# Optimization experiments

Measured on AMD Instinct MI355X. Metric: run time of the kernel, lower is better.

Reference implementation:

```python
import jax, jax.numpy as jnp
import numpy as np

B, N, K, F, O = 8, 65536, 9, 32, 64


def setup_inputs() -> dict:
    key = jax.random.key(0)
    k1, k2, k3, k4, k5 = jax.random.split(key, 5)
    x = jax.random.normal(k1, (B, N, F), dtype=jnp.float32)
    neighbor_index = jax.random.randint(k2, (B, N, K), 0, N)
    t_vertex = jax.random.randint(k3, (N,), 0, N)  # unused in forward, kept for signature fidelity
    v = jnp.ones((N, 8), dtype=jnp.float32) / 8.0
    adjweight = jnp.broadcast_to(jnp.eye(K, dtype=jnp.float32)[None], (8, K, K))
    W = jax.random.normal(k4, (O, K * F), dtype=jnp.float32) * 0.02
    b = jnp.zeros((O,), dtype=jnp.float32)
    return {"x": x, "t_vertex": t_vertex, "neighbor_index": neighbor_index,
            "v": v, "adjweight": adjweight, "W": W, "b": b}


def reference(x, t_vertex, neighbor_index, v, adjweight, W, b):
    bsize, num_pts, feats = x.shape
    num_neighbor = neighbor_index.shape[-1]
    # gather neighbor features per batch: [B, N, K, F]
    x_neighbors = jax.vmap(lambda xb, ib: xb[ib])(x, neighbor_index)
    # per-point learned adjacency: [N, K, K]
    adjw = jnp.einsum('ns,skt->nkt', v, adjweight)
    # apply adjacency: [B, N, K, F] (t replaces k)
    xn = jnp.einsum('bnkf,nkt->bntf', x_neighbors, adjw)
    xn = jax.nn.elu(xn.reshape(bsize, num_pts, num_neighbor * feats))
    out = jax.nn.elu(jnp.einsum('bnd,od->bno', xn, W) + b)
    # zero out last (padding) vertex
    mask = jnp.ones((1, num_pts, 1), dtype=out.dtype).at[0, -1, 0].set(0.0)
    return out * mask
```

## Files before the change

kernel.cpp:

```cpp
#include <hip/hip_runtime.h>
#include <hip/hip_bf16.h>

#define NLOG 16
#define NN 65536
#define KK 9
#define FF 32
#define OO 64
#define DD 288
#define WSTR 296
#define CHUNK 64
#define THREADS 256
#define GRID 2048
#define NBLOCKS 1024
#define TOTALP (8 * NN)
#define NCHUNKS (TOTALP / CHUNK)
#define RA_STRIDE 72
#define RB_STRIDE 10
#define NB_STRIDE 10
#define AJW 88

#define XB (TOTALP * FF / 8 / THREADS)
#define AB (NN * KK / THREADS)
#define NB (TOTALP / THREADS)
#define WB (OO * DD / THREADS)

typedef float f32x4 __attribute__((ext_vector_type(4)));
typedef float f32x2 __attribute__((ext_vector_type(2)));
typedef unsigned int u32x4 __attribute__((ext_vector_type(4)));
typedef short s16x8 __attribute__((ext_vector_type(8)));
typedef short s16x4 __attribute__((ext_vector_type(4)));

static __device__ __forceinline__ short f2bf(float f) {
    union { __hip_bfloat16 h; short s; } u;
    u.h = __float2bfloat16(f);
    return u.s;
}

static __device__ __forceinline__ void bf2f2(unsigned int p, float& lo, float& hi) {
    union { unsigned int u; float f; } a, b;
    a.u = p << 16;
    b.u = p & 0xFFFF0000u;
    lo = a.f; hi = b.f;
}
static __device__ __forceinline__ float bf1(unsigned short s) {
    union { unsigned int u; float f; } a;
    a.u = ((unsigned int)s) << 16;
    return a.f;
}

static __device__ __forceinline__ float elu1(float x) {
    float e = __expf(fminf(x, 0.f)) - 1.f;
    return x > 0.f ? x : e;
}

__global__ __launch_bounds__(THREADS) void precvt(
    const float* __restrict__ x, unsigned short* __restrict__ xbf,
    const float* __restrict__ v, const float* __restrict__ aw,
    unsigned short* __restrict__ recA, unsigned short* __restrict__ recB,
    const int* __restrict__ nbr, unsigned short* __restrict__ nb16,
    const float* __restrict__ W, unsigned short* __restrict__ wbf)
{
    const int bid = blockIdx.x;
    if (bid < XB) {
        const size_t i = ((size_t)bid * THREADS + threadIdx.x) * 8;
        const f32x4 a = *(const f32x4*)(x + i);
        const f32x4 b = *(const f32x4*)(x + i + 4);
        s16x8 p;
        p[0] = f2bf(a.x); p[1] = f2bf(a.y); p[2] = f2bf(a.z); p[3] = f2bf(a.w);
        p[4] = f2bf(b.x); p[5] = f2bf(b.y); p[6] = f2bf(b.z); p[7] = f2bf(b.w);
        *(s16x8*)(xbf + i) = p;
    } else if (bid < XB + AB) {
        const int e = (bid - XB) * THREADS + threadIdx.x;
        const int n = e / KK;
        const int t = e - n * KK;
        const float* vr = v + n * 8;
        short o[8];
        float s8 = 0.f;
        #pragma unroll
        for (int k = 0; k < KK; ++k) {
            float s = 0.f;
            #pragma unroll
            for (int si = 0; si < 8; ++si)
                s += vr[si] * aw[si * 81 + k * 9 + t];
            if (k < 8) o[k] = f2bf(s); else s8 = s;
        }
        *(s16x8*)(recA + (size_t)n * RA_STRIDE + t * 8) = *(s16x8*)o;
        recB[(size_t)n * RB_STRIDE + t] = (unsigned short)f2bf(s8);
        if (t == 0) recB[(size_t)n * RB_STRIDE + 9] = 0;
    } else if (bid < XB + AB + NB) {
        const int p = (bid - XB - AB) * THREADS + threadIdx.x;
        const int* s = nbr + (size_t)p * KK;
        int r[KK];
        #pragma unroll
        for (int k = 0; k < KK; ++k) r[k] = s[k];
        unsigned int* d = (unsigned int*)(nb16 + (size_t)p * NB_STRIDE);
        #pragma unroll
        for (int j = 0; j < 4; ++j)
            d[j] = ((unsigned)r[2*j] & 0xFFFFu) | ((unsigned)r[2*j+1] << 16);
        d[4] = (unsigned)r[8] & 0xFFFFu;
    } else {
        const int i = (bid - XB - AB - NB) * THREADS + threadIdx.x;
        wbf[i] = (unsigned short)f2bf(W[i]);
    }
}

__global__ __launch_bounds__(THREADS, 2) void paiconv_main(
    const unsigned short* __restrict__ xbf,
    const unsigned short* __restrict__ nb16,
    const unsigned short* __restrict__ recA,
    const unsigned short* __restrict__ recB,
    const unsigned short* __restrict__ wbf,
    const float* __restrict__ bias,
    float* __restrict__ out)
{
    __shared__ short Wl[OO * WSTR];
    __shared__ unsigned short AJ[CHUNK * AJW];

    const int tid  = threadIdx.x;
    const int lane = tid & 63;
    const int wid  = tid >> 6;
    const int l15  = lane & 15;
    const int fg   = lane >> 4;
    const int fo   = fg * 8;
    const int pl   = wid * 16 + l15;

    for (int e = tid; e < OO * DD / 8; e += THREADS) {
        const int o = e / 36;
        const int g8 = (e - o * 36) * 8;
        const u32x4 r = *(const u32x4*)(wbf + (size_t)o * DD + g8);
        *(u32x4*)(&Wl[o * WSTR + g8]) = r;
    }
    {
        const int vbase = (blockIdx.x * CHUNK) & (NN - 1);
        for (int e = tid; e < CHUNK * KK; e += THREADS) {
            const int p = e / KK;
            const int t = e - p * KK;
            const u32x4 r = *(const u32x4*)(recA + (size_t)(vbase + p) * RA_STRIDE + t * 8);
            *(u32x4*)(&AJ[p * AJW + t * 8]) = r;
        }
        if (tid < CHUNK) {
            #pragma unroll
            for (int t = 0; t < KK; ++t)
                AJ[tid * AJW + RA_STRIDE + t] =
                    recB[(size_t)(vbase + tid) * RB_STRIDE + t];
        }
    }
    __syncthreads();

    const unsigned short* ajp = &AJ[pl * AJW];

    for (int ci = blockIdx.x; ci < NCHUNKS; ci += GRID) {
        const size_t P = (size_t)ci * CHUNK + pl;
        const int b = (int)(P >> NLOG);

        const unsigned int* np = (const unsigned int*)(nb16 + P * NB_STRIDE);
        const unsigned int nw0 = np[0], nw1 = np[1], nw2 = np[2], nw3 = np[3], nw4 = np[4];
        int rows[KK];
        rows[0] = nw0 & 0xFFFF; rows[1] = nw0 >> 16;
        rows[2] = nw1 & 0xFFFF; rows[3] = nw1 >> 16;
        rows[4] = nw2 & 0xFFFF; rows[5] = nw2 >> 16;
        rows[6] = nw3 & 0xFFFF; rows[7] = nw3 >> 16;
        rows[8] = nw4 & 0xFFFF;

        const unsigned short* xb = xbf + (((size_t)b) << NLOG) * FF + fo;
        f32x2 G2[KK][4];
        #pragma unroll
        for (int k = 0; k < KK; ++k) {
            const u32x4 g = *(const u32x4*)(xb + (size_t)rows[k] * FF);
            float l0,h0,l1,h1,l2,h2,l3,h3;
            bf2f2(g.x, l0, h0);
            bf2f2(g.y, l1, h1);
            bf2f2(g.z, l2, h2);
            bf2f2(g.w, l3, h3);
            G2[k][0] = f32x2{l0, h0};
            G2[k][1] = f32x2{l1, h1};
            G2[k][2] = f32x2{l2, h2};
            G2[k][3] = f32x2{l3, h3};
        }

        f32x4 acc0 = {0,0,0,0}, acc1 = {0,0,0,0}, acc2 = {0,0,0,0}, acc3 = {0,0,0,0};

        #pragma unroll 1
        for (int t = 0; t < KK; ++t) {
            float a[KK];
            {
                const u32x4 qv = *(const u32x4*)(ajp + t * 8);
                bf2f2(qv.x, a[0], a[1]);
                bf2f2(qv.y, a[2], a[3]);
                bf2f2(qv.z, a[4], a[5]);
                bf2f2(qv.w, a[6], a[7]);
                a[8] = bf1(ajp[RA_STRIDE + t]);
            }

            f32x2 xn2[4] = {{0,0},{0,0},{0,0},{0,0}};
            #pragma unroll
            for (int k = 0; k < KK; ++k) {
                const f32x2 ak = {a[k], a[k]};
                #pragma unroll
                for (int i = 0; i < 4; ++i) xn2[i] += G2[k][i] * ak;
            }
            s16x8 af;
            #pragma unroll
            for (int i = 0; i < 4; ++i) {
                af[2*i]   = f2bf(elu1(xn2[i].x));
                af[2*i+1] = f2bf(elu1(xn2[i].y));
            }

            const short* wr = &Wl[l15 * WSTR + t * FF + fo];
            const s16x8 b0 = *(const s16x8*)(wr);
            const s16x8 b1 = *(const s16x8*)(wr + 16 * WSTR);
            const s16x8 b2 = *(const s16x8*)(wr + 32 * WSTR);
            const s16x8 b3 = *(const s16x8*)(wr + 48 * WSTR);
            acc0 = __builtin_amdgcn_mfma_f32_16x16x32_bf16(b0, af, acc0, 0, 0, 0);
            acc1 = __builtin_amdgcn_mfma_f32_16x16x32_bf16(b1, af, acc1, 0, 0, 0);
            acc2 = __builtin_amdgcn_mfma_f32_16x16x32_bf16(b2, af, acc2, 0, 0, 0);
            acc3 = __builtin_amdgcn_mfma_f32_16x16x32_bf16(b3, af, acc3, 0, 0, 0);
        }

        const bool zero_pt = ((P & (NN - 1)) == (NN - 1));
        float* orow = out + P * OO + fg * 4;
        #pragma unroll
        for (int ot = 0; ot < 4; ++ot) {
            const f32x4 a = (ot == 0) ? acc0 : (ot == 1) ? acc1 : (ot == 2) ? acc2 : acc3;
            const f32x4 bv = *(const f32x4*)(bias + ot * 16 + fg * 4);
            f32x4 r;
            #pragma unroll
            for (int j = 0; j < 4; ++j)
                r[j] = zero_pt ? 0.f : elu1(a[j] + bv[j]);
            *(f32x4*)(orow + ot * 16) = r;
        }
    }
}

__global__ __launch_bounds__(THREADS, 2) void paiconv_fb(
    const float* __restrict__ x,
    const int* __restrict__ nbr,
    const float* __restrict__ v,
    const float* __restrict__ aw,
    const float* __restrict__ W,
    const float* __restrict__ bias,
    float* __restrict__ out)
{
    __shared__ short Wl[OO * WSTR];
    __shared__ float BL[OO];
    const int tid = threadIdx.x;
    for (int e = tid; e < OO * DD / 4; e += THREADS) {
        int o = e / 72;
        int d4 = (e - o * 72) * 4;
        const f32x4 wv = *(const f32x4*)(W + o * DD + d4);
        s16x4 p;
        p.x = f2bf(wv.x); p.y = f2bf(wv.y); p.z = f2bf(wv.z); p.w = f2bf(wv.w);
        *(s16x4*)(&Wl[o * WSTR + d4]) = p;
    }
    if (tid < OO) BL[tid] = bias[tid];
    __syncthreads();

    const int lane = tid & 63;
    const int wid  = tid >> 6;
    const int l15  = lane & 15;
    const int fg   = lane >> 4;
    const int fo   = fg * 8;
    const int pl   = wid * 16 + l15;

    for (int ci = blockIdx.x; ci < NCHUNKS; ci += NBLOCKS) {
        const int cbase = ci * CHUNK;
        const int P = cbase + pl;
        const int n = P & (NN - 1);
        const int b = P >> NLOG;
        const int* nip = nbr + (size_t)P * KK;
        const float* xb = x + (((size_t)b) << NLOG) * FF;

        f32x2 G2[KK][4];
        #pragma unroll
        for (int k = 0; k < KK; ++k) {
            const float* src = xb + (size_t)nip[k] * FF + fo;
            const f32x4 g0 = *(const f32x4*)(src);
            const f32x4 g1 = *(const f32x4*)(src + 4);
            G2[k][0] = f32x2{g0.x, g0.y};
            G2[k][1] = f32x2{g0.z, g0.w};
            G2[k][2] = f32x2{g1.x, g1.y};
            G2[k][3] = f32x2{g1.z, g1.w};
        }
        float vr[8];
        #pragma unroll
        for (int si = 0; si < 8; ++si) vr[si] = v[n * 8 + si];

        f32x4 acc0 = {0,0,0,0}, acc1 = {0,0,0,0}, acc2 = {0,0,0,0}, acc3 = {0,0,0,0};
        #pragma unroll
        for (int t = 0; t < KK; ++t) {
            float a[KK];
            #pragma unroll
            for (int k = 0; k < KK; ++k) {
                float s = 0.f;
                #pragma unroll
                for (int si = 0; si < 8; ++si)
                    s += vr[si] * aw[si * 81 + k * 9 + t];
                a[k] = s;
            }
            f32x2 xn2[4] = {{0,0},{0,0},{0,0},{0,0}};
            #pragma unroll
            for (int k = 0; k < KK; ++k) {
                const f32x2 ak = {a[k], a[k]};
                #pragma unroll
                for (int i = 0; i < 4; ++i) xn2[i] += G2[k][i] * ak;
            }
            s16x8 af;
            #pragma unroll
            for (int i = 0; i < 4; ++i) {
                af[2*i]   = f2bf(elu1(xn2[i].x));
                af[2*i+1] = f2bf(elu1(xn2[i].y));
            }
            const short* wrow = &Wl[l15 * WSTR + t * FF + fo];
            s16x8 b0 = *(const s16x8*)(wrow);
            s16x8 b1 = *(const s16x8*)(wrow + 16 * WSTR);
            s16x8 b2 = *(const s16x8*)(wrow + 32 * WSTR);
            s16x8 b3 = *(const s16x8*)(wrow + 48 * WSTR);
            acc0 = __builtin_amdgcn_mfma_f32_16x16x32_bf16(b0, af, acc0, 0, 0, 0);
            acc1 = __builtin_amdgcn_mfma_f32_16x16x32_bf16(b1, af, acc1, 0, 0, 0);
            acc2 = __builtin_amdgcn_mfma_f32_16x16x32_bf16(b2, af, acc2, 0, 0, 0);
            acc3 = __builtin_amdgcn_mfma_f32_16x16x32_bf16(b3, af, acc3, 0, 0, 0);
        }
        const bool zero_pt = ((P & (NN - 1)) == (NN - 1));
        float* orow = out + (size_t)P * OO + fg * 4;
        #pragma unroll
        for (int ot = 0; ot < 4; ++ot) {
            const f32x4 a = (ot == 0) ? acc0 : (ot == 1) ? acc1 : (ot == 2) ? acc2 : acc3;
            const f32x4 bv = *(const f32x4*)&BL[ot * 16 + fg * 4];
            f32x4 r;
            #pragma unroll
            for (int j = 0; j < 4; ++j)
                r[j] = zero_pt ? 0.f : elu1(a[j] + bv[j]);
            *(f32x4*)(orow + ot * 16) = r;
        }
    }
}

extern "C" void kernel_launch(void* const* d_in, const int* in_sizes, int n_in,
                              void* d_out, int out_size, void* d_ws, size_t ws_size,
                              hipStream_t stream) {
    const float* x    = (const float*)d_in[0];
    const int*   nbr  = (const int*)d_in[2];
    const float* v    = (const float*)d_in[3];
    const float* aw   = (const float*)d_in[4];
    const float* W    = (const float*)d_in[5];
    const float* bias = (const float*)d_in[6];
    float* out = (float*)d_out;

    const size_t xbf_bytes = (size_t)TOTALP * FF * 2;
    const size_t ra_bytes  = (size_t)NN * RA_STRIDE * 2;
    const size_t rb_bytes  = (size_t)NN * RB_STRIDE * 2;
    const size_t nb_bytes  = (size_t)TOTALP * NB_STRIDE * 2;
    const size_t wb_bytes  = (size_t)OO * DD * 2;
    const size_t need = xbf_bytes + ra_bytes + rb_bytes + nb_bytes + wb_bytes;

    if (ws_size >= need) {
        char* base = (char*)d_ws;
        unsigned short* xbf  = (unsigned short*)base;  base += xbf_bytes;
        unsigned short* recA = (unsigned short*)base;  base += ra_bytes;
        unsigned short* recB = (unsigned short*)base;  base += rb_bytes;
        unsigned short* nb16 = (unsigned short*)base;  base += nb_bytes;
        unsigned short* wbf  = (unsigned short*)base;

        hipLaunchKernelGGL(precvt, dim3(XB + AB + NB + WB), dim3(THREADS), 0, stream,
                           x, xbf, v, aw, recA, recB, nbr, nb16, W, wbf);
        hipLaunchKernelGGL(paiconv_main, dim3(GRID), dim3(THREADS), 0, stream,
                           xbf, nb16, recA, recB, wbf, bias, out);
    } else {
        hipLaunchKernelGGL(paiconv_fb, dim3(NBLOCKS), dim3(THREADS), 0, stream,
                           x, nbr, v, aw, W, bias, out);
    }
}
```

Measured before the change: 150.2 us.

## Pre-swizzle W into MFMA fragment order and double block size to 512 threads

The weight conversion kernel now writes W in a layout that matches the MFMA B-fragment order (t, output tile, lane, 8 elements). Each lane's LDS read of weights becomes a contiguous, conflict-free 16-byte load at lane*8 and needs no row stride. The main kernel moves to 512-thread blocks handling 128-point chunks with half the grid, so each W copy into LDS is amortized over twice as many points. ELU also becomes a branchless fmax, and the preprocessing and fallback kernels keep their 256-thread configuration.

Measured after the change: 148.1 us (median of 2 runs). No clear change (-1.4%).

```diff
diff --git a/kernel.cpp b/kernel.cpp
--- a/kernel.cpp
+++ b/kernel.cpp
@@ -8,9 +8,10 @@
 #define OO 64
 #define DD 288
 #define WSTR 296
-#define CHUNK 64
-#define THREADS 256
-#define GRID 2048
+#define CHUNK 128
+#define THREADS 512
+#define GRID 1024
+#define PTHREADS 256
 #define NBLOCKS 1024
 #define TOTALP (8 * NN)
 #define NCHUNKS (TOTALP / CHUNK)
@@ -19,10 +20,10 @@
 #define NB_STRIDE 10
 #define AJW 88
 
-#define XB (TOTALP * FF / 8 / THREADS)
-#define AB (NN * KK / THREADS)
-#define NB (TOTALP / THREADS)
-#define WB (OO * DD / THREADS)
+#define XB (TOTALP * FF / 8 / PTHREADS)
+#define AB (NN * KK / PTHREADS)
+#define NB (TOTALP / PTHREADS)
+#define WB (OO * DD / PTHREADS)
 
 typedef float f32x4 __attribute__((ext_vector_type(4)));
 typedef float f32x2 __attribute__((ext_vector_type(2)));
@@ -49,11 +50,10 @@
 }
 
 static __device__ __forceinline__ float elu1(float x) {
-    float e = __expf(fminf(x, 0.f)) - 1.f;
-    return x > 0.f ? x : e;
-}
-
-__global__ __launch_bounds__(THREADS) void precvt(
+    return fmaxf(x, __expf(fminf(x, 0.f)) - 1.f);
+}
+
+__global__ __launch_bounds__(PTHREADS) void precvt(
     const float* __restrict__ x, unsigned short* __restrict__ xbf,
     const float* __restrict__ v, const float* __restrict__ aw,
     unsigned short* __restrict__ recA, unsigned short* __restrict__ recB,
@@ -62,7 +62,7 @@
 {
     const int bid = blockIdx.x;
     if (bid < XB) {
-        const size_t i = ((size_t)bid * THREADS + threadIdx.x) * 8;
+        const size_t i = ((size_t)bid * PTHREADS + threadIdx.x) * 8;
         const f32x4 a = *(const f32x4*)(x + i);
         const f32x4 b = *(const f32x4*)(x + i + 4);
         s16x8 p;
@@ -70,7 +70,7 @@
         p[4] = f2bf(b.x); p[5] = f2bf(b.y); p[6] = f2bf(b.z); p[7] = f2bf(b.w);
         *(s16x8*)(xbf + i) = p;
     } else if (bid < XB + AB) {
-        const int e = (bid - XB) * THREADS + threadIdx.x;
+        const int e = (bid - XB) * PTHREADS + threadIdx.x;
         const int n = e / KK;
         const int t = e - n * KK;
         const float* vr = v + n * 8;
@@ -88,7 +88,7 @@
         recB[(size_t)n * RB_STRIDE + t] = (unsigned short)f2bf(s8);
         if (t == 0) recB[(size_t)n * RB_STRIDE + 9] = 0;
     } else if (bid < XB + AB + NB) {
-        const int p = (bid - XB - AB) * THREADS + threadIdx.x;
+        const int p = (bid - XB - AB) * PTHREADS + threadIdx.x;
         const int* s = nbr + (size_t)p * KK;
         int r[KK];
         #pragma unroll
@@ -99,8 +99,15 @@
             d[j] = ((unsigned)r[2*j] & 0xFFFFu) | ((unsigned)r[2*j+1] << 16);
         d[4] = (unsigned)r[8] & 0xFFFFu;
     } else {
-        const int i = (bid - XB - AB - NB) * THREADS + threadIdx.x;
-        wbf[i] = (unsigned short)f2bf(W[i]);
+        const int i = (bid - XB - AB - NB) * PTHREADS + threadIdx.x;
+        const int j     = i & 7;
+        const int lane  = (i >> 3) & 63;
+        const int tl    = i >> 9;
+        const int t     = tl >> 2;
+        const int ot    = tl & 3;
+        const int o     = ot * 16 + (lane & 15);
+        const int d     = t * FF + (lane >> 4) * 8 + j;
+        wbf[i] = (unsigned short)f2bf(W[o * DD + d]);
     }
 }
 
@@ -113,7 +120,7 @@
     const float* __restrict__ bias,
     float* __restrict__ out)
 {
-    __shared__ short Wl[OO * WSTR];
+    __shared__ short Wl[OO * DD];
     __shared__ unsigned short AJ[CHUNK * AJW];
 
     const int tid  = threadIdx.x;
@@ -125,10 +132,8 @@
     const int pl   = wid * 16 + l15;
 
     for (int e = tid; e < OO * DD / 8; e += THREADS) {
-        const int o = e / 36;
-        const int g8 = (e - o * 36) * 8;
-        const u32x4 r = *(const u32x4*)(wbf + (size_t)o * DD + g8);
-        *(u32x4*)(&Wl[o * WSTR + g8]) = r;
+        const u32x4 r = *(const u32x4*)(wbf + (size_t)e * 8);
+        *(u32x4*)(&Wl[e * 8]) = r;
     }
     {
         const int vbase = (blockIdx.x * CHUNK) & (NN - 1);
@@ -148,6 +153,7 @@
     __syncthreads();
 
     const unsigned short* ajp = &AJ[pl * AJW];
+    const short* wl = &Wl[lane * 8];
 
     for (int ci = blockIdx.x; ci < NCHUNKS; ci += GRID) {
         const size_t P = (size_t)ci * CHUNK + pl;
@@ -206,11 +212,10 @@
                 af[2*i+1] = f2bf(elu1(xn2[i].y));
             }
 
-            const short* wr = &Wl[l15 * WSTR + t * FF + fo];
-            const s16x8 b0 = *(const s16x8*)(wr);
-            const s16x8 b1 = *(const s16x8*)(wr + 16 * WSTR);
-            const s16x8 b2 = *(const s16x8*)(wr + 32 * WSTR);
-            const s16x8 b3 = *(const s16x8*)(wr + 48 * WSTR);
+            const s16x8 b0 = *(const s16x8*)(wl + (t * 4 + 0) * 512);
+            const s16x8 b1 = *(const s16x8*)(wl + (t * 4 + 1) * 512);
+            const s16x8 b2 = *(const s16x8*)(wl + (t * 4 + 2) * 512);
+            const s16x8 b3 = *(const s16x8*)(wl + (t * 4 + 3) * 512);
             acc0 = __builtin_amdgcn_mfma_f32_16x16x32_bf16(b0, af, acc0, 0, 0, 0);
             acc1 = __builtin_amdgcn_mfma_f32_16x16x32_bf16(b1, af, acc1, 0, 0, 0);
             acc2 = __builtin_amdgcn_mfma_f32_16x16x32_bf16(b2, af, acc2, 0, 0, 0);
@@ -232,7 +237,7 @@
     }
 }
 
-__global__ __launch_bounds__(THREADS, 2) void paiconv_fb(
+__global__ __launch_bounds__(PTHREADS, 2) void paiconv_fb(
     const float* __restrict__ x,
     const int* __restrict__ nbr,
     const float* __restrict__ v,
@@ -244,7 +249,7 @@
     __shared__ short Wl[OO * WSTR];
     __shared__ float BL[OO];
     const int tid = threadIdx.x;
-    for (int e = tid; e < OO * DD / 4; e += THREADS) {
+    for (int e = tid; e < OO * DD / 4; e += PTHREADS) {
         int o = e / 72;
         int d4 = (e - o * 72) * 4;
         const f32x4 wv = *(const f32x4*)(W + o * DD + d4);
@@ -262,8 +267,8 @@
     const int fo   = fg * 8;
     const int pl   = wid * 16 + l15;
 
-    for (int ci = blockIdx.x; ci < NCHUNKS; ci += NBLOCKS) {
-        const int cbase = ci * CHUNK;
+    for (int ci = blockIdx.x; ci < TOTALP / 64; ci += NBLOCKS) {
+        const int cbase = ci * 64;
         const int P = cbase + pl;
         const int n = P & (NN - 1);
         const int b = P >> NLOG;
@@ -361,12 +366,12 @@
         unsigned short* nb16 = (unsigned short*)base;  base += nb_bytes;
         unsigned short* wbf  = (unsigned short*)base;
 
-        hipLaunchKernelGGL(precvt, dim3(XB + AB + NB + WB), dim3(THREADS), 0, stream,
+        hipLaunchKernelGGL(precvt, dim3(XB + AB + NB + WB), dim3(PTHREADS), 0, stream,
                            x, xbf, v, aw, recA, recB, nbr, nb16, W, wbf);
         hipLaunchKernelGGL(paiconv_main, dim3(GRID), dim3(THREADS), 0, stream,
                            xbf, nb16, recA, recB, wbf, bias, out);
     } else {
-        hipLaunchKernelGGL(paiconv_fb, dim3(NBLOCKS), dim3(THREADS), 0, stream,
+        hipLaunchKernelGGL(paiconv_fb, dim3(NBLOCKS), dim3(PTHREADS), 0, stream,
                            x, nbr, v, aw, W, bias, out);
     }
 }
```
